# Kernel tuning notes

Hardware: AMD Instinct MI355X
Metric: run time of the kernel (lower is better)

The kernel has to match this reference:

```python
import jax, jax.numpy as jnp
import numpy as np

N, E, F_IN, H, C = 50000, 800000, 128, 4, 73
HC = H * C  # 292
NEG_SLOPE_ATT = 0.2   # GATv2 attention leaky relu
NEG_SLOPE_ACT = 0.01  # F.leaky_relu default
BN_EPS = 1e-5


def setup_inputs() -> dict:
    key = jax.random.key(0)
    ks = jax.random.split(key, 20)
    rn = lambda k, shp, s=0.05: (jax.random.normal(k, shp, jnp.float32) * s)
    inp = {
        'x': jax.random.normal(ks[0], (N, F_IN), jnp.float32),
        'edge_index': jax.random.randint(ks[1], (2, E), 0, N, jnp.int64),
        # conv1 (in=F_IN)
        'Wl1': rn(ks[2], (HC, F_IN)), 'bl1': rn(ks[3], (HC,)),
        'Wr1': rn(ks[4], (HC, F_IN)), 'br1': rn(ks[5], (HC,)),
        'att1': rn(ks[6], (H, C)), 'b1': rn(ks[7], (HC,)),
        # conv2 (in=HC)
        'Wl2': rn(ks[8], (HC, HC)), 'bl2': rn(ks[9], (HC,)),
        'Wr2': rn(ks[10], (HC, HC)), 'br2': rn(ks[11], (HC,)),
        'att2': rn(ks[12], (H, C)), 'b2': rn(ks[13], (HC,)),
        # shared BatchNorm1d(HC)
        'gamma': jnp.ones((HC,), jnp.float32), 'beta': jnp.zeros((HC,), jnp.float32),
        # classifier Linear(HC, 2)
        'Wc': rn(ks[14], (2, HC)), 'bc': rn(ks[15], (2,)),
    }
    return inp


def _gatv2(x, src, dst, Wl, bl, Wr, br, att, b):
    # lin_l on source, lin_r on target (PyG GATv2Conv, share_weights=False)
    xl = (x @ Wl.T + bl).reshape(-1, H, C)  # [N,H,C]
    xr = (x @ Wr.T + br).reshape(-1, H, C)
    f = xl[src] + xr[dst]                    # [E,H,C] edge-wise gather
    s = jnp.einsum('ehc,hc->eh', jax.nn.leaky_relu(f, NEG_SLOPE_ATT), att)
    # segment softmax over incoming edges of each destination node
    m = jax.ops.segment_max(s, dst, num_segments=N)
    ex = jnp.exp(s - m[dst])
    den = jax.ops.segment_sum(ex, dst, num_segments=N)
    alpha = ex / (den[dst] + 1e-16)          # [E,H]
    out = jax.ops.segment_sum(alpha[:, :, None] * xl[src], dst, num_segments=N)
    return out.reshape(-1, HC) + b           # concat heads + bias


def _bn(x, gamma, beta):
    mu = jnp.mean(x, axis=0)
    var = jnp.mean((x - mu) ** 2, axis=0)
    return (x - mu) * jax.lax.rsqrt(var + BN_EPS) * gamma + beta


def reference(x, edge_index, Wl1, bl1, Wr1, br1, att1, b1,
              Wl2, bl2, Wr2, br2, att2, b2, gamma, beta, Wc, bc):
    src, dst = edge_index[0], edge_index[1]
    h = _gatv2(x, src, dst, Wl1, bl1, Wr1, br1, att1, b1)
    h = jax.nn.leaky_relu(_bn(h, gamma, beta), NEG_SLOPE_ACT)
    h = _gatv2(h, src, dst, Wl2, bl2, Wr2, br2, att2, b2)
    h = jax.nn.leaky_relu(_bn(h, gamma, beta), NEG_SLOPE_ACT)
    return h @ Wc.T + bc
```

## Files before the change

### kernel.cpp

```cpp
#include <hip/hip_runtime.h>

#define HCDIM 292
#define NHEAD 4
#define CDIM 73
#define SLOTS 5
#define NPERM 320
#define BN_EPS 1e-5f
#define LOG2E 1.44269504f

using u16x8 = __attribute__((ext_vector_type(8))) unsigned short;
using f32x4 = __attribute__((ext_vector_type(4))) float;
using u16x4 = __attribute__((ext_vector_type(4))) unsigned short;
using hf2   = __attribute__((ext_vector_type(2))) _Float16;
using v2h   = __attribute__((ext_vector_type(2))) __fp16;
using v8h   = __attribute__((ext_vector_type(8))) __fp16;

__device__ inline v2h pkrtz(float a, float b) {
  return __builtin_amdgcn_cvt_pkrtz(a, b);
}
__device__ inline float fdot2(hf2 a, hf2 b, float c) {
  return __builtin_amdgcn_fdot2(__builtin_bit_cast(v2h, a),
                                __builtin_bit_cast(v2h, b), c, false);
}
__device__ inline ushort f2h(float f) {
  _Float16 h = (_Float16)f;
  return __builtin_bit_cast(ushort, h);
}
__device__ inline float h2f(ushort v) {
  return (float)__builtin_bit_cast(_Float16, v);
}
__device__ inline hf2 habs2(hf2 a) {
  unsigned u = __builtin_bit_cast(unsigned, a) & 0x7fff7fffu;
  return __builtin_bit_cast(hf2, u);
}
__device__ inline float fexp2(float x) {
  float r;
  asm("v_exp_f32 %0, %1" : "=v"(r) : "v"(x));
  return r;
}

__device__ inline float dpp16_allsum(float v) {
  union { float f; int i; } a, b;
  a.f = v;
  b.i = __builtin_amdgcn_update_dpp(0, a.i, 0xB1, 0xf, 0xf, true);
  a.f += b.f;
  b.i = __builtin_amdgcn_update_dpp(0, a.i, 0x4E, 0xf, 0xf, true);
  a.f += b.f;
  b.i = __builtin_amdgcn_update_dpp(0, a.i, 0x124, 0xf, 0xf, true);
  a.f += b.f;
  b.i = __builtin_amdgcn_update_dpp(0, a.i, 0x128, 0xf, 0xf, true);
  a.f += b.f;
  return a.f;
}

__device__ inline int perm2feat(int p, bool& valid) {
  int h, c;
  if (p < 256) {
    h = p >> 6;
    c = ((p & 3) << 4) | ((p >> 2) & 15);
    valid = true;
  } else {
    int q = p - 256;
    h = q >> 4;
    c = 64 + (q & 15);
    valid = (q & 15) < (CDIM - 64);
  }
  return h * CDIM + c;
}

__global__ void k_wperm2(const float* __restrict__ W0, const float* __restrict__ b0,
                         const float* __restrict__ W1, const float* __restrict__ b1,
                         ushort* __restrict__ Wp, float* __restrict__ pb,
                         int Kin, int Kpad, int kperm) {
  const float* W = blockIdx.y ? W1 : W0;
  const float* b = blockIdx.y ? b1 : b0;
  ushort* Wpo = Wp + (size_t)blockIdx.y * NPERM * Kpad;
  float* pbo = pb + blockIdx.y * NPERM;
  int p = blockIdx.x, t = threadIdx.x;
  bool pv;
  int gn = perm2feat(p, pv);
  int gk = t;
  bool kv = t < Kin;
  if (kperm) { bool v2; gk = perm2feat(t, v2); kv = v2; }
  ushort v = 0;
  if (pv && kv) v = f2h(W[(size_t)gn * Kin + gk]);
  Wpo[(size_t)p * Kpad + t] = v;
  if (t == 0) pbo[p] = pv ? b[gn] : 0.f;
}

__global__ void k_vecperm(const float* __restrict__ att1, const float* __restrict__ b1,
                          const float* __restrict__ att2, const float* __restrict__ b2,
                          const float* __restrict__ gamma, const float* __restrict__ beta,
                          const float* __restrict__ Wc, float* __restrict__ o) {
  int p = threadIdx.x, w = blockIdx.x;
  bool pv;
  int gn = perm2feat(p, pv);
  const float* src;
  switch (w) {
    case 0: src = att1; break;
    case 1: src = b1; break;
    case 2: src = att2; break;
    case 3: src = b2; break;
    case 4: src = gamma; break;
    case 5: src = beta; break;
    case 6: src = Wc; break;
    default: src = Wc + HCDIM; break;
  }
  o[w * NPERM + p] = pv ? src[gn] : 0.f;
}

__global__ void k_hist(const int* __restrict__ dst, int* __restrict__ deg, int E) {
  int i = blockIdx.x * blockDim.x + threadIdx.x;
  if (i < E) atomicAdd(&deg[dst[i]], 1);
}

__global__ __launch_bounds__(256) void k_block_sum(const int* __restrict__ deg,
                                                   int* __restrict__ bsum, int n) {
  __shared__ int s[256];
  int i = blockIdx.x * 256 + threadIdx.x;
  s[threadIdx.x] = (i < n) ? deg[i] : 0;
  __syncthreads();
  for (int off = 128; off > 0; off >>= 1) {
    if (threadIdx.x < off) s[threadIdx.x] += s[threadIdx.x + off];
    __syncthreads();
  }
  if (threadIdx.x == 0) bsum[blockIdx.x] = s[0];
}

__global__ __launch_bounds__(256) void k_scan_small(const int* __restrict__ bsum,
                                                    int* __restrict__ boff, int G) {
  __shared__ int s[256];
  int t = threadIdx.x;
  int v = (t < G) ? bsum[t] : 0;
  s[t] = v;
  __syncthreads();
  for (int off = 1; off < 256; off <<= 1) {
    int tv = (t >= off) ? s[t - off] : 0;
    __syncthreads();
    s[t] += tv;
    __syncthreads();
  }
  if (t < G) boff[t] = s[t] - v;
}

__global__ __launch_bounds__(256) void k_scan_final(const int* __restrict__ deg,
                                                    const int* __restrict__ boff,
                                                    int* __restrict__ row_ptr,
                                                    int* __restrict__ cursor,
                                                    int n, int E) {
  __shared__ int s[256];
  int t = threadIdx.x;
  int i = blockIdx.x * 256 + t;
  int v = (i < n) ? deg[i] : 0;
  s[t] = v;
  __syncthreads();
  for (int off = 1; off < 256; off <<= 1) {
    int tv = (t >= off) ? s[t - off] : 0;
    __syncthreads();
    s[t] += tv;
    __syncthreads();
  }
  if (i < n) {
    int rp = boff[blockIdx.x] + s[t] - v;
    row_ptr[i] = rp;
    cursor[i] = rp;
  }
  if (i == 0) row_ptr[n] = E;
}

__global__ void k_csr_fill(const int* __restrict__ srcs, const int* __restrict__ dsts,
                           int* __restrict__ cursor, int* __restrict__ csr_src, int E) {
  int i = blockIdx.x * blockDim.x + threadIdx.x;
  if (i < E) {
    int pos = atomicAdd(&cursor[dsts[i]], 1);
    csr_src[pos] = srcs[i];
  }
}

template <int KS, int MODE>
__global__ __launch_bounds__(256, 4) void k_gemm_a_lds(
    const void* __restrict__ Av, const ushort* __restrict__ Wb,
    const float* __restrict__ pb, const float* __restrict__ bnscale,
    const float* __restrict__ bnshift, ushort* __restrict__ o0,
    ushort* __restrict__ o1, int M) {
  constexpr int KSTEPS = KS / 32;
  constexpr int STR = KS + 8;
  __shared__ ushort As[64 * STR];
  const int tid = threadIdx.x;
  const int rbase = blockIdx.x * 64;
  const int y = blockIdx.y;
  const int wave = tid >> 6, lane = tid & 63;
  const int quad = lane >> 4, lr = lane & 15;
  const int ct = wave;

  if constexpr (MODE == 0) {
    const float* X = (const float*)Av;
    constexpr int NIT = (64 * KS / 16) / 256;
#pragma unroll
    for (int k = 0; k < NIT; ++k) {
      int idx = tid + k * 256;
      int row = idx >> 3, sg = idx & 7;
      int gr = rbase + row;
      if (gr >= M) gr = M - 1;
      const float4* p = (const float4*)(X + (size_t)gr * KS + sg * 16);
      float4 f0 = p[0], f1 = p[1], f2 = p[2], f3 = p[3];
      union { v2h h[4]; u16x8 v; } a, b;
      a.h[0] = pkrtz(f0.x, f0.y); a.h[1] = pkrtz(f0.z, f0.w);
      a.h[2] = pkrtz(f1.x, f1.y); a.h[3] = pkrtz(f1.z, f1.w);
      b.h[0] = pkrtz(f2.x, f2.y); b.h[1] = pkrtz(f2.z, f2.w);
      b.h[2] = pkrtz(f3.x, f3.y); b.h[3] = pkrtz(f3.z, f3.w);
      *(u16x8*)(As + row * STR + sg * 16) = a.v;
      *(u16x8*)(As + row * STR + sg * 16 + 8) = b.v;
    }
  } else {
    const ushort* Hn = (const ushort*)Av;
    constexpr int NIT = (64 * KS / 8) / 256;
#pragma unroll
    for (int k = 0; k < NIT; ++k) {
      int idx = tid + k * 256;
      int row = idx / (KS / 8), c8 = idx - row * (KS / 8);
      int gr = rbase + row;
      if (gr >= M) gr = M - 1;
      u16x8 v = *(const u16x8*)(Hn + (size_t)gr * KS + c8 * 8);
      int c = c8 * 8;
      float4 s0 = *(const float4*)(bnscale + c);
      float4 s1 = *(const float4*)(bnscale + c + 4);
      float4 t0 = *(const float4*)(bnshift + c);
      float4 t1 = *(const float4*)(bnshift + c + 4);
      float f[8];
      f[0] = fmaf(h2f(v[0]), s0.x, t0.x);
      f[1] = fmaf(h2f(v[1]), s0.y, t0.y);
      f[2] = fmaf(h2f(v[2]), s0.z, t0.z);
      f[3] = fmaf(h2f(v[3]), s0.w, t0.w);
      f[4] = fmaf(h2f(v[4]), s1.x, t1.x);
      f[5] = fmaf(h2f(v[5]), s1.y, t1.y);
      f[6] = fmaf(h2f(v[6]), s1.z, t1.z);
      f[7] = fmaf(h2f(v[7]), s1.w, t1.w);
#pragma unroll
      for (int j = 0; j < 8; ++j) f[j] = (f[j] > 0.f) ? f[j] : 0.01f * f[j];
      union { v2h h4[4]; u16x8 o; } u;
#pragma unroll
      for (int j = 0; j < 4; ++j) u.h4[j] = pkrtz(f[2 * j], f[2 * j + 1]);
      *(u16x8*)(As + row * STR + c8 * 8) = u.o;
    }
  }
  __syncthreads();

  const ushort* bcol[5];
#pragma unroll
  for (int i = 0; i < 5; ++i)
    bcol[i] = Wb + (size_t)(y * 320 + ct * 80 + i * 16 + lr) * KS;
  const ushort* arow[4];
#pragma unroll
  for (int i = 0; i < 4; ++i) arow[i] = As + (i * 16 + lr) * STR;

  f32x4 acc[4][5] = {};
#pragma unroll
  for (int s = 0; s < KSTEPS; ++s) {
    v8h bf[5], af[4];
#pragma unroll
    for (int i = 0; i < 5; ++i)
      bf[i] = *(const v8h*)(bcol[i] + s * 32 + quad * 8);
#pragma unroll
    for (int i = 0; i < 4; ++i)
      af[i] = *(const v8h*)(arow[i] + s * 32 + quad * 8);
#pragma unroll
    for (int ni = 0; ni < 5; ++ni)
#pragma unroll
      for (int mi = 0; mi < 4; ++mi)
        acc[mi][ni] = __builtin_amdgcn_mfma_f32_16x16x32_f16(
            bf[ni], af[mi], acc[mi][ni], 0, 0, 0);
  }

  ushort* out = y ? o1 : o0;
  const int colbase = ct * 80;
  float4 pbv[5];
#pragma unroll
  for (int ni = 0; ni < 5; ++ni)
    pbv[ni] = *(const float4*)(pb + y * 320 + ct * 80 + ni * 16 + quad * 4);
#pragma unroll
  for (int mi = 0; mi < 4; ++mi) {
    int gm = rbase + mi * 16 + lr;
    if (gm >= M) continue;
    ushort* orow = out + (size_t)gm * NPERM + colbase + quad * 4;
#pragma unroll
    for (int ni = 0; ni < 5; ++ni) {
      union { v2h h[2]; u16x4 o; } u;
      u.h[0] = pkrtz(acc[mi][ni][0] + pbv[ni].x, acc[mi][ni][1] + pbv[ni].y);
      u.h[1] = pkrtz(acc[mi][ni][2] + pbv[ni].z, acc[mi][ni][3] + pbv[ni].w);
      *(u16x4*)(orow + ni * 16) = u.o;
    }
  }
}

__global__ __launch_bounds__(256) void k_pre(const ushort* __restrict__ xl,
                                             const float* __restrict__ attp,
                                             float* __restrict__ pl, int n) {
  int wave = threadIdx.x >> 6, lane = threadIdx.x & 63;
  int d = blockIdx.x * 4 + wave;
  if (d >= n) return;
  int hgrp = lane >> 4, li = lane & 15;
  const float C = 0.4f * LOG2E;
  float4 a4 = *(const float4*)(attp + lane * 4);
  hf2 av01{(_Float16)(C * a4.x), (_Float16)(C * a4.y)};
  hf2 av23{(_Float16)(C * a4.z), (_Float16)(C * a4.w)};
  hf2 av5{(_Float16)(C * attp[256 + lane]), (_Float16)0.f};

  uint2 cc = *(const uint2*)(xl + (size_t)d * NPERM + lane * 4);
  ushort c5 = xl[(size_t)d * NPERM + 256 + lane];
  hf2 c01 = __builtin_bit_cast(hf2, cc.x);
  hf2 c23 = __builtin_bit_cast(hf2, cc.y);
  hf2 c5h{__builtin_bit_cast(_Float16, c5), (_Float16)0.f};

  float Ta = fdot2(c01, av01, fdot2(c23, av23, fdot2(c5h, av5, 0.f)));
  Ta = dpp16_allsum(Ta);
  if (li == 0) pl[d * 4 + hgrp] = 1.5f * Ta;
}

__global__ __launch_bounds__(128) void k_agg(const ushort* __restrict__ xl,
                                             const ushort* __restrict__ xr,
                                             const float* __restrict__ pl,
                                             const int* __restrict__ csr_src,
                                             const int* __restrict__ row_ptr,
                                             const float* __restrict__ attp,
                                             const float* __restrict__ bp,
                                             ushort* __restrict__ out, int n) {
  int wave = threadIdx.x >> 6, lane = threadIdx.x & 63;
  int d = blockIdx.x * 2 + wave;
  if (d >= n) return;
  int hgrp = lane >> 4;
  int start = __builtin_amdgcn_readfirstlane(row_ptr[d]);
  int end = __builtin_amdgcn_readfirstlane(row_ptr[d + 1]);

  float4 bp4 = *(const float4*)(bp + lane * 4);
  float bp5 = bp[256 + lane];

  if (start >= end) {
    union { v2h h[2]; u16x4 o; } u;
    u.h[0] = pkrtz(bp4.x, bp4.y);
    u.h[1] = pkrtz(bp4.z, bp4.w);
    *(u16x4*)(out + (size_t)d * NPERM + lane * 4) = u.o;
    out[(size_t)d * NPERM + 256 + lane] = f2h(bp5);
    return;
  }

  const float C = 0.4f * LOG2E;
  float4 at4 = *(const float4*)(attp + lane * 4);
  hf2 av01{(_Float16)(C * at4.x), (_Float16)(C * at4.y)};
  hf2 av23{(_Float16)(C * at4.z), (_Float16)(C * at4.w)};
  hf2 av5{(_Float16)(C * attp[256 + lane]), (_Float16)0.f};

  hf2 xr01, xr23, xr5;
  {
    uint2 rr = *(const uint2*)(xr + (size_t)d * NPERM + lane * 4);
    xr01 = __builtin_bit_cast(hf2, rr.x);
    xr23 = __builtin_bit_cast(hf2, rr.y);
    xr5 = hf2{__builtin_bit_cast(_Float16, xr[(size_t)d * NPERM + 256 + lane]),
              (_Float16)0.f};
  }
  float Tb = fdot2(xr01, av01, fdot2(xr23, av23, fdot2(xr5, av5, 0.f)));
  Tb = dpp16_allsum(Tb);
  float prv = 1.5f * Tb;
  float acc[SLOTS] = {};
  float den = 0.f;
  int dg = end - start;
  int nfull = dg >> 2;
  int rem = dg & 3;

  uint2 s8[4];
  ushort s1[4];
  float spv[4];
#pragma unroll
  for (int k = 0; k < 4; ++k) {
    int e = start + k;
    if (e > end - 1) e = end - 1;
    int s = __builtin_amdgcn_readfirstlane(csr_src[e]);
    s8[k] = *(const uint2*)(xl + (size_t)s * NPERM + lane * 4);
    s1[k] = xl[(size_t)s * NPERM + 256 + lane];
    spv[k] = pl[s * 4 + hgrp] + prv;
  }

  for (int g = 0; g < nfull; ++g) {
    int ebase = start + g * 4 + 4;
    uint2 n8[4];
    ushort n1[4];
    float np[4];
#pragma unroll
    for (int k = 0; k < 4; ++k) {
      int e = ebase + k;
      if (e > end - 1) e = end - 1;
      int s = __builtin_amdgcn_readfirstlane(csr_src[e]);
      n8[k] = *(const uint2*)(xl + (size_t)s * NPERM + lane * 4);
      n1[k] = xl[(size_t)s * NPERM + 256 + lane];
      np[k] = pl[s * 4 + hgrp] + prv;
    }

    hf2 x01[4], x23[4], x5[4];
    float T[4];
#pragma unroll
    for (int k = 0; k < 4; ++k) {
      x01[k] = __builtin_bit_cast(hf2, s8[k].x);
      x23[k] = __builtin_bit_cast(hf2, s8[k].y);
      x5[k] = hf2{__builtin_bit_cast(_Float16, s1[k]), (_Float16)0.f};
      T[k] = fdot2(habs2(x01[k] + xr01), av01,
             fdot2(habs2(x23[k] + xr23), av23,
             fdot2(habs2(x5[k] + xr5), av5, 0.f)));
    }
#pragma unroll
    for (int k = 0; k < 4; ++k) T[k] = dpp16_allsum(T[k]);
    float w[4];
#pragma unroll
    for (int k = 0; k < 4; ++k) {
      w[k] = fexp2(fminf(T[k] + spv[k], 80.f));
      den += w[k];
    }
#pragma unroll
    for (int k = 0; k < 4; ++k) {
      acc[0] = fmaf(w[k], (float)x01[k][0], acc[0]);
      acc[1] = fmaf(w[k], (float)x01[k][1], acc[1]);
      acc[2] = fmaf(w[k], (float)x23[k][0], acc[2]);
      acc[3] = fmaf(w[k], (float)x23[k][1], acc[3]);
      acc[4] = fmaf(w[k], (float)x5[k][0], acc[4]);
    }
#pragma unroll
    for (int k = 0; k < 4; ++k) { s8[k] = n8[k]; s1[k] = n1[k]; spv[k] = np[k]; }
  }

#pragma unroll
  for (int k = 0; k < 3; ++k) {
    if (k < rem) {
      hf2 x01 = __builtin_bit_cast(hf2, s8[k].x);
      hf2 x23 = __builtin_bit_cast(hf2, s8[k].y);
      hf2 x5{__builtin_bit_cast(_Float16, s1[k]), (_Float16)0.f};
      float T = fdot2(habs2(x01 + xr01), av01,
                fdot2(habs2(x23 + xr23), av23,
                fdot2(habs2(x5 + xr5), av5, 0.f)));
      T = dpp16_allsum(T);
      float w = fexp2(fminf(T + spv[k], 80.f));
      den += w;
      acc[0] = fmaf(w, (float)x01[0], acc[0]);
      acc[1] = fmaf(w, (float)x01[1], acc[1]);
      acc[2] = fmaf(w, (float)x23[0], acc[2]);
      acc[3] = fmaf(w, (float)x23[1], acc[3]);
      acc[4] = fmaf(w, (float)x5[0], acc[4]);
    }
  }

  float inv = 1.f / (den + 1e-16f);
  union { v2h h[2]; u16x4 o; } u;
  u.h[0] = pkrtz(fmaf(acc[0], inv, bp4.x), fmaf(acc[1], inv, bp4.y));
  u.h[1] = pkrtz(fmaf(acc[2], inv, bp4.z), fmaf(acc[3], inv, bp4.w));
  *(u16x4*)(out + (size_t)d * NPERM + lane * 4) = u.o;
  out[(size_t)d * NPERM + 256 + lane] = f2h(fmaf(acc[4], inv, bp5));
}

__global__ __launch_bounds__(320) void k_bn_reduce(const ushort* __restrict__ h,
                                                   float* __restrict__ colsum,
                                                   float* __restrict__ colsq,
                                                   int n, int rows_per_block) {
  int c = threadIdx.x;
  int r0 = blockIdx.x * rows_per_block;
  int r1 = min(r0 + rows_per_block, n);
  float s = 0.f, s2 = 0.f;
  for (int r = r0; r < r1; ++r) {
    float v = h2f(h[(size_t)r * NPERM + c]);
    s += v;
    s2 += v * v;
  }
  atomicAdd(&colsum[c], s);
  atomicAdd(&colsq[c], s2);
}

__global__ void k_bn_coef(float* __restrict__ colsum, float* __restrict__ colsq,
                          const float* __restrict__ gp, const float* __restrict__ bp,
                          float invN) {
  int c = threadIdx.x + blockIdx.x * blockDim.x;
  if (c >= NPERM) return;
  float mu = colsum[c] * invN;
  float var = colsq[c] * invN - mu * mu;
  float scale = rsqrtf(var + BN_EPS) * gp[c];
  colsum[c] = scale;
  colsq[c] = bp[c] - mu * scale;
}

__global__ __launch_bounds__(256) void k_bn_classifier(
    const ushort* __restrict__ h, const float* __restrict__ scale,
    const float* __restrict__ shift, const float* __restrict__ wc0,
    const float* __restrict__ wc1, const float* __restrict__ bc,
    float* __restrict__ out, int n) {
  int wave = threadIdx.x >> 6, lane = threadIdx.x & 63;
  int r = blockIdx.x * 4 + wave;
  if (r >= n) return;
  float a0 = 0.f, a1 = 0.f;
#pragma unroll
  for (int k = 0; k < SLOTS; ++k) {
    int slot = lane + 64 * k;
    float v = fmaf(h2f(h[(size_t)r * NPERM + slot]), scale[slot], shift[slot]);
    v = (v > 0.f) ? v : 0.01f * v;
    a0 = fmaf(v, wc0[slot], a0);
    a1 = fmaf(v, wc1[slot], a1);
  }
#pragma unroll
  for (int off = 32; off > 0; off >>= 1) {
    a0 += __shfl_xor(a0, off, 64);
    a1 += __shfl_xor(a1, off, 64);
  }
  if (lane == 0) {
    out[(size_t)2 * r] = a0 + bc[0];
    out[(size_t)2 * r + 1] = a1 + bc[1];
  }
}

extern "C" void kernel_launch(void* const* d_in, const int* in_sizes, int n_in,
                              void* d_out, int out_size, void* d_ws, size_t ws_size,
                              hipStream_t stream) {
  const float* x      = (const float*)d_in[0];
  const int*   eidx   = (const int*)d_in[1];
  const float* Wl1    = (const float*)d_in[2];
  const float* bl1    = (const float*)d_in[3];
  const float* Wr1    = (const float*)d_in[4];
  const float* br1    = (const float*)d_in[5];
  const float* att1   = (const float*)d_in[6];
  const float* b1     = (const float*)d_in[7];
  const float* Wl2    = (const float*)d_in[8];
  const float* bl2    = (const float*)d_in[9];
  const float* Wr2    = (const float*)d_in[10];
  const float* br2    = (const float*)d_in[11];
  const float* att2   = (const float*)d_in[12];
  const float* b2     = (const float*)d_in[13];
  const float* gamma  = (const float*)d_in[14];
  const float* beta   = (const float*)d_in[15];
  const float* Wc     = (const float*)d_in[16];
  const float* bc     = (const float*)d_in[17];
  float* out = (float*)d_out;

  const int FIN = 128;
  const int N = in_sizes[0] / FIN;
  const int E = in_sizes[1] / 2;

  const int* src = eidx;
  const int* dst = eidx + E;

  ushort* h      = (ushort*)d_ws;
  ushort* xl     = h + (size_t)N * NPERM;
  ushort* xr     = xl + (size_t)N * NPERM;
  ushort* abuf   = xr + (size_t)N * NPERM;
  ushort* wb     = abuf + (size_t)N * NPERM;
  float* pb      = (float*)(wb + (size_t)2 * NPERM * NPERM);
  float* vecp    = pb + 2 * NPERM;
  float* pl      = vecp + 8 * NPERM;
  float* colsum  = pl + (size_t)N * NHEAD;
  float* colsq   = colsum + NPERM;
  int* deg       = (int*)(colsq + NPERM);
  int* row_ptr   = deg + N;
  int* cursor    = row_ptr + N + 1;
  int* bsum      = cursor + N;
  int* boff      = bsum + 256;
  int* csr_src   = boff + 256;

  const int G = (N + 255) / 256;
  const int EB = (E + 255) / 256;
  const int AGGB = (N + 3) / 4;
  const int AGG2 = (N + 1) / 2;
  const dim3 GEMMG((N + 63) / 64, 2);

  const float* att1p = vecp;
  const float* b1p   = vecp + NPERM;
  const float* att2p = vecp + 2 * NPERM;
  const float* b2p   = vecp + 3 * NPERM;
  const float* gp    = vecp + 4 * NPERM;
  const float* btp   = vecp + 5 * NPERM;
  const float* wc0   = vecp + 6 * NPERM;
  const float* wc1   = vecp + 7 * NPERM;

  hipMemsetAsync(deg, 0, (size_t)N * sizeof(int), stream);
  k_hist<<<EB, 256, 0, stream>>>(dst, deg, E);
  k_block_sum<<<G, 256, 0, stream>>>(deg, bsum, N);
  k_scan_small<<<1, 256, 0, stream>>>(bsum, boff, G);
  k_scan_final<<<G, 256, 0, stream>>>(deg, boff, row_ptr, cursor, N, E);
  k_csr_fill<<<EB, 256, 0, stream>>>(src, dst, cursor, csr_src, E);

  k_vecperm<<<8, NPERM, 0, stream>>>(att1, b1, att2, b2, gamma, beta, Wc, vecp);

  k_wperm2<<<dim3(NPERM, 2), FIN, 0, stream>>>(Wl1, bl1, Wr1, br1, wb, pb,
                                               FIN, FIN, 0);
  k_gemm_a_lds<128, 0><<<GEMMG, 256, 0, stream>>>((const void*)x, wb, pb,
                                                  nullptr, nullptr, xl, xr, N);
  k_pre<<<AGGB, 256, 0, stream>>>(xl, att1p, pl, N);
  k_agg<<<AGG2, 128, 0, stream>>>(xl, xr, pl, csr_src, row_ptr, att1p, b1p, h, N);

  const int BNB = 1024;
  const int RPB = (N + BNB - 1) / BNB;
  hipMemsetAsync(colsum, 0, 2 * NPERM * sizeof(float), stream);
  k_bn_reduce<<<BNB, NPERM, 0, stream>>>(h, colsum, colsq, N, RPB);
  k_bn_coef<<<2, 160, 0, stream>>>(colsum, colsq, gp, btp, 1.f / (float)N);

  k_wperm2<<<dim3(NPERM, 2), NPERM, 0, stream>>>(Wl2, bl2, Wr2, br2, wb, pb,
                                                 HCDIM, NPERM, 1);
  k_gemm_a_lds<NPERM, 1><<<GEMMG, 256, 0, stream>>>((const void*)h, wb, pb,
                                                    colsum, colsq, xl, xr, N);
  k_pre<<<AGGB, 256, 0, stream>>>(xl, att2p, pl, N);
  k_agg<<<AGG2, 128, 0, stream>>>(xl, xr, pl, csr_src, row_ptr, att2p, b2p, h, N);

  hipMemsetAsync(colsum, 0, 2 * NPERM * sizeof(float), stream);
  k_bn_reduce<<<BNB, NPERM, 0, stream>>>(h, colsum, colsq, N, RPB);
  k_bn_coef<<<2, 160, 0, stream>>>(colsum, colsq, gp, btp, 1.f / (float)N);

  k_bn_classifier<<<AGGB, 256, 0, stream>>>(h, colsum, colsq, wc0, wc1, bc, out, N);
}
```

Baseline: 578.1 us.

## Fuse GEMM halves into one block and compute source attention term inline

The GEMM kernel now computes both the xl and xr outputs in a single block by looping over y, so the A tile staged into LDS is loaded and converted once instead of twice. The separate k_pre kernel that precomputed the per-source linear attention term is removed. k_agg now recomputes that term per edge from the gathered xl values using extra fdot2 and DPP reductions. This trades extra ALU work per edge in aggregation for one fewer kernel launch and no pl array traffic, and it halves the GEMM grid, which may reduce parallelism.

Result: faster. 546.1 us (-5.5%).

```diff
diff --git a/kernel.cpp b/kernel.cpp
--- a/kernel.cpp
+++ b/kernel.cpp
@@ -188,7 +188,6 @@
   __shared__ ushort As[64 * STR];
   const int tid = threadIdx.x;
   const int rbase = blockIdx.x * 64;
-  const int y = blockIdx.y;
   const int wave = tid >> 6, lane = tid & 63;
   const int quad = lane >> 4, lr = lane & 15;
   const int ct = wave;
@@ -246,80 +245,59 @@
   }
   __syncthreads();
 
-  const ushort* bcol[5];
-#pragma unroll
-  for (int i = 0; i < 5; ++i)
-    bcol[i] = Wb + (size_t)(y * 320 + ct * 80 + i * 16 + lr) * KS;
   const ushort* arow[4];
 #pragma unroll
   for (int i = 0; i < 4; ++i) arow[i] = As + (i * 16 + lr) * STR;
 
-  f32x4 acc[4][5] = {};
-#pragma unroll
-  for (int s = 0; s < KSTEPS; ++s) {
-    v8h bf[5], af[4];
+#pragma unroll
+  for (int y = 0; y < 2; ++y) {
+    const ushort* bcol[5];
 #pragma unroll
     for (int i = 0; i < 5; ++i)
-      bf[i] = *(const v8h*)(bcol[i] + s * 32 + quad * 8);
-#pragma unroll
-    for (int i = 0; i < 4; ++i)
-      af[i] = *(const v8h*)(arow[i] + s * 32 + quad * 8);
+      bcol[i] = Wb + (size_t)(y * 320 + ct * 80 + i * 16 + lr) * KS;
+
+    f32x4 acc[4][5] = {};
+#pragma unroll
+    for (int s = 0; s < KSTEPS; ++s) {
+      v8h bf[5], af[4];
+#pragma unroll
+      for (int i = 0; i < 5; ++i)
+        bf[i] = *(const v8h*)(bcol[i] + s * 32 + quad * 8);
+#pragma unroll
+      for (int i = 0; i < 4; ++i)
+        af[i] = *(const v8h*)(arow[i] + s * 32 + quad * 8);
+#pragma unroll
+      for (int ni = 0; ni < 5; ++ni)
+#pragma unroll
+        for (int mi = 0; mi < 4; ++mi)
+          acc[mi][ni] = __builtin_amdgcn_mfma_f32_16x16x32_f16(
+              bf[ni], af[mi], acc[mi][ni], 0, 0, 0);
+    }
+
+    ushort* out = y ? o1 : o0;
+    const int colbase = ct * 80;
+    float4 pbv[5];
 #pragma unroll
     for (int ni = 0; ni < 5; ++ni)
-#pragma unroll
-      for (int mi = 0; mi < 4; ++mi)
-        acc[mi][ni] = __builtin_amdgcn_mfma_f32_16x16x32_f16(
-            bf[ni], af[mi], acc[mi][ni], 0, 0, 0);
-  }
-
-  ushort* out = y ? o1 : o0;
-  const int colbase = ct * 80;
-  float4 pbv[5];
-#pragma unroll
-  for (int ni = 0; ni < 5; ++ni)
-    pbv[ni] = *(const float4*)(pb + y * 320 + ct * 80 + ni * 16 + quad * 4);
-#pragma unroll
-  for (int mi = 0; mi < 4; ++mi) {
-    int gm = rbase + mi * 16 + lr;
-    if (gm >= M) continue;
-    ushort* orow = out + (size_t)gm * NPERM + colbase + quad * 4;
-#pragma unroll
-    for (int ni = 0; ni < 5; ++ni) {
-      union { v2h h[2]; u16x4 o; } u;
-      u.h[0] = pkrtz(acc[mi][ni][0] + pbv[ni].x, acc[mi][ni][1] + pbv[ni].y);
-      u.h[1] = pkrtz(acc[mi][ni][2] + pbv[ni].z, acc[mi][ni][3] + pbv[ni].w);
-      *(u16x4*)(orow + ni * 16) = u.o;
-    }
-  }
-}
-
-__global__ __launch_bounds__(256) void k_pre(const ushort* __restrict__ xl,
-                                             const float* __restrict__ attp,
-                                             float* __restrict__ pl, int n) {
-  int wave = threadIdx.x >> 6, lane = threadIdx.x & 63;
-  int d = blockIdx.x * 4 + wave;
-  if (d >= n) return;
-  int hgrp = lane >> 4, li = lane & 15;
-  const float C = 0.4f * LOG2E;
-  float4 a4 = *(const float4*)(attp + lane * 4);
-  hf2 av01{(_Float16)(C * a4.x), (_Float16)(C * a4.y)};
-  hf2 av23{(_Float16)(C * a4.z), (_Float16)(C * a4.w)};
-  hf2 av5{(_Float16)(C * attp[256 + lane]), (_Float16)0.f};
-
-  uint2 cc = *(const uint2*)(xl + (size_t)d * NPERM + lane * 4);
-  ushort c5 = xl[(size_t)d * NPERM + 256 + lane];
-  hf2 c01 = __builtin_bit_cast(hf2, cc.x);
-  hf2 c23 = __builtin_bit_cast(hf2, cc.y);
-  hf2 c5h{__builtin_bit_cast(_Float16, c5), (_Float16)0.f};
-
-  float Ta = fdot2(c01, av01, fdot2(c23, av23, fdot2(c5h, av5, 0.f)));
-  Ta = dpp16_allsum(Ta);
-  if (li == 0) pl[d * 4 + hgrp] = 1.5f * Ta;
+      pbv[ni] = *(const float4*)(pb + y * 320 + ct * 80 + ni * 16 + quad * 4);
+#pragma unroll
+    for (int mi = 0; mi < 4; ++mi) {
+      int gm = rbase + mi * 16 + lr;
+      if (gm >= M) continue;
+      ushort* orow = out + (size_t)gm * NPERM + colbase + quad * 4;
+#pragma unroll
+      for (int ni = 0; ni < 5; ++ni) {
+        union { v2h h[2]; u16x4 o; } u;
+        u.h[0] = pkrtz(acc[mi][ni][0] + pbv[ni].x, acc[mi][ni][1] + pbv[ni].y);
+        u.h[1] = pkrtz(acc[mi][ni][2] + pbv[ni].z, acc[mi][ni][3] + pbv[ni].w);
+        *(u16x4*)(orow + ni * 16) = u.o;
+      }
+    }
+  }
 }
 
 __global__ __launch_bounds__(128) void k_agg(const ushort* __restrict__ xl,
                                              const ushort* __restrict__ xr,
-                                             const float* __restrict__ pl,
                                              const int* __restrict__ csr_src,
                                              const int* __restrict__ row_ptr,
                                              const float* __restrict__ attp,
@@ -328,7 +306,6 @@
   int wave = threadIdx.x >> 6, lane = threadIdx.x & 63;
   int d = blockIdx.x * 2 + wave;
   if (d >= n) return;
-  int hgrp = lane >> 4;
   int start = __builtin_amdgcn_readfirstlane(row_ptr[d]);
   int end = __builtin_amdgcn_readfirstlane(row_ptr[d + 1]);
 
@@ -369,7 +346,6 @@
 
   uint2 s8[4];
   ushort s1[4];
-  float spv[4];
 #pragma unroll
   for (int k = 0; k < 4; ++k) {
     int e = start + k;
@@ -377,14 +353,12 @@
     int s = __builtin_amdgcn_readfirstlane(csr_src[e]);
     s8[k] = *(const uint2*)(xl + (size_t)s * NPERM + lane * 4);
     s1[k] = xl[(size_t)s * NPERM + 256 + lane];
-    spv[k] = pl[s * 4 + hgrp] + prv;
   }
 
   for (int g = 0; g < nfull; ++g) {
     int ebase = start + g * 4 + 4;
     uint2 n8[4];
     ushort n1[4];
-    float np[4];
 #pragma unroll
     for (int k = 0; k < 4; ++k) {
       int e = ebase + k;
@@ -392,11 +366,10 @@
       int s = __builtin_amdgcn_readfirstlane(csr_src[e]);
       n8[k] = *(const uint2*)(xl + (size_t)s * NPERM + lane * 4);
       n1[k] = xl[(size_t)s * NPERM + 256 + lane];
-      np[k] = pl[s * 4 + hgrp] + prv;
     }
 
     hf2 x01[4], x23[4], x5[4];
-    float T[4];
+    float T[4], Tl[4];
 #pragma unroll
     for (int k = 0; k < 4; ++k) {
       x01[k] = __builtin_bit_cast(hf2, s8[k].x);
@@ -405,13 +378,20 @@
       T[k] = fdot2(habs2(x01[k] + xr01), av01,
              fdot2(habs2(x23[k] + xr23), av23,
              fdot2(habs2(x5[k] + xr5), av5, 0.f)));
-    }
-#pragma unroll
-    for (int k = 0; k < 4; ++k) T[k] = dpp16_allsum(T[k]);
+      Tl[k] = fdot2(x01[k], av01, fdot2(x23[k], av23, fdot2(x5[k], av5, 0.f)));
+    }
+#pragma unroll
+    for (int k = 0; k < 4; ++k) {
+      T[k] = dpp16_allsum(T[k]);
+      Tl[k] = dpp16_allsum(Tl[k]);
+    }
     float w[4];
 #pragma unroll
     for (int k = 0; k < 4; ++k) {
-      w[k] = fexp2(fminf(T[k] + spv[k], 80.f));
+      float plv = 1.5f * Tl[k];
+      asm("" : "+v"(plv));
+      float spv = plv + prv;
+      w[k] = fexp2(fminf(T[k] + spv, 80.f));
       den += w[k];
     }
 #pragma unroll
@@ -423,7 +403,7 @@
       acc[4] = fmaf(w[k], (float)x5[k][0], acc[4]);
     }
 #pragma unroll
-    for (int k = 0; k < 4; ++k) { s8[k] = n8[k]; s1[k] = n1[k]; spv[k] = np[k]; }
+    for (int k = 0; k < 4; ++k) { s8[k] = n8[k]; s1[k] = n1[k]; }
   }
 
 #pragma unroll
@@ -435,8 +415,12 @@
       float T = fdot2(habs2(x01 + xr01), av01,
                 fdot2(habs2(x23 + xr23), av23,
                 fdot2(habs2(x5 + xr5), av5, 0.f)));
+      float Tl = fdot2(x01, av01, fdot2(x23, av23, fdot2(x5, av5, 0.f)));
       T = dpp16_allsum(T);
-      float w = fexp2(fminf(T + spv[k], 80.f));
+      Tl = dpp16_allsum(Tl);
+      float plv = 1.5f * Tl;
+      asm("" : "+v"(plv));
+      float w = fexp2(fminf(T + (plv + prv), 80.f));
       den += w;
       acc[0] = fmaf(w, (float)x01[0], acc[0]);
       acc[1] = fmaf(w, (float)x01[1], acc[1]);
@@ -562,7 +546,7 @@
   const int EB = (E + 255) / 256;
   const int AGGB = (N + 3) / 4;
   const int AGG2 = (N + 1) / 2;
-  const dim3 GEMMG((N + 63) / 64, 2);
+  const int GEMMB = (N + 63) / 64;
 
   const float* att1p = vecp;
   const float* b1p   = vecp + NPERM;
@@ -584,10 +568,9 @@
 
   k_wperm2<<<dim3(NPERM, 2), FIN, 0, stream>>>(Wl1, bl1, Wr1, br1, wb, pb,
                                                FIN, FIN, 0);
-  k_gemm_a_lds<128, 0><<<GEMMG, 256, 0, stream>>>((const void*)x, wb, pb,
+  k_gemm_a_lds<128, 0><<<GEMMB, 256, 0, stream>>>((const void*)x, wb, pb,
                                                   nullptr, nullptr, xl, xr, N);
-  k_pre<<<AGGB, 256, 0, stream>>>(xl, att1p, pl, N);
-  k_agg<<<AGG2, 128, 0, stream>>>(xl, xr, pl, csr_src, row_ptr, att1p, b1p, h, N);
+  k_agg<<<AGG2, 128, 0, stream>>>(xl, xr, csr_src, row_ptr, att1p, b1p, h, N);
 
   const int BNB = 1024;
   const int RPB = (N + BNB - 1) / BNB;
@@ -597,10 +580,9 @@
 
   k_wperm2<<<dim3(NPERM, 2), NPERM, 0, stream>>>(Wl2, bl2, Wr2, br2, wb, pb,
                                                  HCDIM, NPERM, 1);
-  k_gemm_a_lds<NPERM, 1><<<GEMMG, 256, 0, stream>>>((const void*)h, wb, pb,
+  k_gemm_a_lds<NPERM, 1><<<GEMMB, 256, 0, stream>>>((const void*)h, wb, pb,
                                                     colsum, colsq, xl, xr, N);
-  k_pre<<<AGGB, 256, 0, stream>>>(xl, att2p, pl, N);
-  k_agg<<<AGG2, 128, 0, stream>>>(xl, xr, pl, csr_src, row_ptr, att2p, b2p, h, N);
+  k_agg<<<AGG2, 128, 0, stream>>>(xl, xr, csr_src, row_ptr, att2p, b2p, h, N);
 
   hipMemsetAsync(colsum, 0, 2 * NPERM * sizeof(float), stream);
   k_bn_reduce<<<BNB, NPERM, 0, stream>>>(h, colsum, colsq, N, RPB);
```
